# Kernel optimization log

Hardware: AMD Instinct MI355X
Metric: run time of the kernel (lower is better)

Reference implementation:

```python
import jax, jax.numpy as jnp
import numpy as np
from jax import lax

R_WIN = 1
WIN = 2 * R_WIN + 1        # 3
K = WIN * WIN              # 9
STRIDE = 4
LATENT = 128
N_LVL = 2


def _conv_relu(x, w, b):
    # x: (B*S, 3, H, W), w: (128, 3, 7, 7) -> (B*S, 128, H/4, W/4)
    y = lax.conv_general_dilated(x, w, (STRIDE, STRIDE), [(3, 3), (3, 3)],
                                 dimension_numbers=('NCHW', 'OIHW', 'NCHW'))
    return jax.nn.relu(y + b[None, :, None, None])


def _bilinear_sample(fmap, gx, gy):
    # fmap (B,C,H,W); gx,gy (B,P) in [-1,1]; align_corners=True, zeros padding
    B, C, H, W = fmap.shape
    ix = (gx + 1.0) * 0.5 * (W - 1)
    iy = (gy + 1.0) * 0.5 * (H - 1)
    x0 = jnp.floor(ix); y0 = jnp.floor(iy)
    x1 = x0 + 1.0;      y1 = y0 + 1.0
    wx1 = ix - x0; wx0 = 1.0 - wx1
    wy1 = iy - y0; wy0 = 1.0 - wy1

    fm_flat = fmap.reshape(B, C, H * W)

    def corner(xf, yf, wgt):
        valid = (xf >= 0) & (xf <= W - 1) & (yf >= 0) & (yf <= H - 1)
        xi = jnp.clip(xf, 0, W - 1).astype(jnp.int32)
        yi = jnp.clip(yf, 0, H - 1).astype(jnp.int32)
        idx = yi * W + xi                              # (B,P)
        g = jax.vmap(lambda fm, ii: fm[:, ii])(fm_flat, idx)  # (B,C,P)
        return g * (wgt * valid)[:, None, :]

    return (corner(x0, y0, wx0 * wy0) + corner(x1, y0, wx1 * wy0)
            + corner(x0, y1, wx0 * wy1) + corner(x1, y1, wx1 * wy1))


def _sample_features(fmap, pts):
    B, C, H, W = fmap.shape
    N = pts.shape[1]
    lin = jnp.linspace(-R_WIN, R_WIN, WIN)
    dy, dx = jnp.meshgrid(lin, lin, indexing='ij')
    off = jnp.stack([dx / (W - 1) * 2.0, dy / (H - 1) * 2.0], -1).reshape(-1, 2)  # (K,2)
    grid = (pts * 2.0 - 1.0)[:, :, None, :] + off[None, None]   # (B,N,K,2)
    grid = grid.reshape(B, N * K, 2)
    s = _bilinear_sample(fmap, grid[..., 0], grid[..., 1])       # (B,C,N*K)
    return s.reshape(B, C, N, WIN, WIN)


def _l2norm(x, axis):
    return x / jnp.maximum(jnp.linalg.norm(x, axis=axis, keepdims=True), 1e-12)


def _forward(queries, frames, conv_w, conv_b, w1, b1, wp, bp, wv, bv):
    B, S, C, H, W = frames.shape
    N = queries.shape[1]
    x = 2.0 * (frames / 255.0) - 1.0
    fm = _conv_relu(x.reshape(B * S, C, H, W), conv_w, conv_b)
    fm = fm.reshape(B, S, LATENT, H // STRIDE, W // STRIDE)

    pyr = [fm]
    for _ in range(N_LVL - 1):
        fm = lax.reduce_window(fm, 0.0, lax.add, (1, 1, 1, WIN, WIN),
                               (1, 1, 1, WIN, WIN), 'VALID') / float(WIN * WIN)
        pyr.append(fm)

    cur = queries                                   # pred_pos aliases queries in torch
    vis_acc = jnp.zeros((B, N), queries.dtype)
    for i in range(N_LVL):
        f5 = pyr[N_LVL - 1 - i]                     # (B,S,C,h,w) coarse -> fine
        feats = _sample_features(f5[:, 0], cur).reshape(B, LATENT, N, K)
        matches = _sample_features(f5[:, 1], cur).reshape(B, LATENT, N, K)
        fn = _l2norm(feats, 1)
        mn = _l2norm(matches, 1)
        corr = jnp.einsum('bcnh,bcnk->bnhk', fn, mn).reshape(B * N, K * K)
        h = jax.nn.relu(corr @ w1 + b1)
        pred = jax.nn.softmax(h @ wp + bp, axis=-1).reshape(B, N, WIN, WIN)
        vis = jax.nn.sigmoid(h @ wv + bv).reshape(B, N)
        hh, ww = f5.shape[3], f5.shape[4]
        dsx = jnp.linspace(-R_WIN / (ww - 1), R_WIN / (ww - 1), WIN)
        dsy = jnp.linspace(-R_WIN / (hh - 1), R_WIN / (hh - 1), WIN)
        d_x = pred.sum(-1) @ dsx                    # (B,N)
        d_y = pred.sum(-2) @ dsy                    # (B,N)
        cur = jnp.stack([cur[..., 0] + d_x, cur[..., 1] + d_y], -1)
        vis_acc = vis_acc + vis
    return cur, vis_acc / float(N_LVL)


def setup_inputs() -> dict:
    key = jax.random.key(0)
    ks = jax.random.split(key, 8)
    B, S, N, H, W = 2, 2, 8192, 384, 512
    return {
        'queries': jax.random.uniform(ks[0], (B, N, 2), jnp.float32),
        'frames': jax.random.uniform(ks[1], (B, S, 3, H, W), jnp.float32) * 255.0,
        'conv_w': jax.random.normal(ks[2], (128, 3, 7, 7), jnp.float32) * 0.02,
        'conv_b': jnp.zeros((128,), jnp.float32),
        'w1': jax.random.normal(ks[3], (81, 256), jnp.float32) * 0.05,
        'b1': jnp.zeros((256,), jnp.float32),
        'wp': jax.random.normal(ks[4], (256, 9), jnp.float32) * 0.05,
        'bp': jnp.zeros((9,), jnp.float32),
        'wv': jax.random.normal(ks[5], (256, 1), jnp.float32) * 0.05,
        'bv': jnp.zeros((1,), jnp.float32),
    }


def reference(queries, frames, conv_w, conv_b, w1, b1, wp, bp, wv, bv):
    return _forward(queries, frames, conv_w, conv_b, w1, b1, wp, bp, wv, bv)
```

## Files before the change

kernel.cpp:

```cpp
#include <hip/hip_runtime.h>
#include <math.h>

#define NQ 8192
#define NP 16384
#define H_IN 384
#define W_IN 512
#define HH0 96
#define WW0 128
#define HH1 32
#define WW1 42

__global__ void transpose_w_kernel(const float* __restrict__ w, float* __restrict__ wT) {
    int idx = blockIdx.x * 256 + threadIdx.x;
    if (idx < 147 * 128) {
        int tap = idx >> 7;
        int oc  = idx & 127;
        wT[idx] = w[oc * 147 + tap];
    }
}

__global__ __launch_bounds__(256) void conv_kernel(
    const float* __restrict__ frames, const float* __restrict__ wT,
    const float* __restrict__ bias, float* __restrict__ out)
{
    __shared__ float lds[3 * 7 * 260];
    const int bs  = blockIdx.z;
    const int oh  = blockIdx.y;
    const int ow0 = blockIdx.x * 64;
    const int tid = threadIdx.x;

    for (int idx = tid; idx < 3 * 7 * 259; idx += 256) {
        int c   = idx / 1813;
        int rem = idx - c * 1813;
        int kh  = rem / 259;
        int col = rem - kh * 259;
        int gy  = oh * 4 - 3 + kh;
        int gx  = ow0 * 4 - 3 + col;
        float v = 0.0f;
        if (gy >= 0 && gy < H_IN && gx >= 0 && gx < W_IN) {
            float t = frames[((size_t)(bs * 3 + c) * H_IN + gy) * W_IN + gx];
            v = 2.0f * (t / 255.0f) - 1.0f;
        }
        lds[c * 1820 + kh * 260 + col] = v;
    }
    __syncthreads();

    const int oc = tid & 63;
    const int g  = tid >> 6;
    float a0[16], a1[16];
#pragma unroll
    for (int p = 0; p < 16; ++p) { a0[p] = 0.0f; a1[p] = 0.0f; }

#pragma unroll
    for (int c = 0; c < 3; ++c) {
#pragma unroll
        for (int kh = 0; kh < 7; ++kh) {
            const float* row = lds + c * 1820 + kh * 260 + g * 64;
            float w0[7], w1v[7];
#pragma unroll
            for (int kw = 0; kw < 7; ++kw) {
                int tap = (c * 7 + kh) * 7 + kw;
                w0[kw]  = wT[tap * 128 + oc];
                w1v[kw] = wT[tap * 128 + oc + 64];
            }
#pragma unroll
            for (int p = 0; p < 16; ++p) {
                const float4 A  = *(const float4*)(row + p * 4);
                const float4 Bv = *(const float4*)(row + p * 4 + 4);
                float s0 = a0[p], s1 = a1[p];
                s0 = fmaf(A.x,  w0[0], s0);  s1 = fmaf(A.x,  w1v[0], s1);
                s0 = fmaf(A.y,  w0[1], s0);  s1 = fmaf(A.y,  w1v[1], s1);
                s0 = fmaf(A.z,  w0[2], s0);  s1 = fmaf(A.z,  w1v[2], s1);
                s0 = fmaf(A.w,  w0[3], s0);  s1 = fmaf(A.w,  w1v[3], s1);
                s0 = fmaf(Bv.x, w0[4], s0);  s1 = fmaf(Bv.x, w1v[4], s1);
                s0 = fmaf(Bv.y, w0[5], s0);  s1 = fmaf(Bv.y, w1v[5], s1);
                s0 = fmaf(Bv.z, w0[6], s0);  s1 = fmaf(Bv.z, w1v[6], s1);
                a0[p] = s0; a1[p] = s1;
            }
        }
    }

    const float b0  = bias[oc];
    const float b1b = bias[oc + 64];
#pragma unroll
    for (int p = 0; p < 16; ++p) {
        int ow = ow0 + g * 16 + p;
        size_t ob = ((size_t)(bs * HH0 + oh) * WW0 + ow) * 128;
        out[ob + oc]      = fmaxf(a0[p] + b0, 0.0f);
        out[ob + oc + 64] = fmaxf(a1[p] + b1b, 0.0f);
    }
}

__global__ void pool_kernel(const float* __restrict__ in, float* __restrict__ out) {
    int idx = blockIdx.x * 256 + threadIdx.x;
    if (idx >= 4 * HH1 * WW1 * 128) return;
    int c = idx & 127;
    int r = idx >> 7;
    int px = r % WW1; r /= WW1;
    int py = r % HH1;
    int bs = r / HH1;
    float s = 0.0f;
#pragma unroll
    for (int dy = 0; dy < 3; ++dy)
#pragma unroll
        for (int dx = 0; dx < 3; ++dx)
            s += in[(((size_t)bs * HH0 + py * 3 + dy) * WW0 + px * 3 + dx) * 128 + c];
    out[idx] = s / 9.0f;
}

__global__ __launch_bounds__(512) void sample_kernel(
    const float* __restrict__ fm, int hh, int ww,
    const float* __restrict__ cur_in, float* __restrict__ corr_out)
{
    __shared__ float smem[4 * 2400];
    const int tid  = threadIdx.x;
    const int wvi  = tid >> 6;
    const int lane = tid & 63;
    const int ps   = wvi >> 1;
    const int mp   = wvi & 1;
    const int p    = blockIdx.x * 4 + ps;
    const int b    = p >> 13;

    float* fl    = smem + ps * 2400;
    float* ml    = fl + 1188;
    float* inv_s = fl + 2376;

    const float2 pxy = *(const float2*)(cur_in + (size_t)p * 2);
    const float wwm1 = (float)(ww - 1);
    const float hhm1 = (float)(hh - 1);
    const float ix = ((pxy.x * 2.0f - 1.0f) + 1.0f) * 0.5f * wwm1;
    const float iy = ((pxy.y * 2.0f - 1.0f) + 1.0f) * 0.5f * hhm1;
    const float x0 = floorf(ix), y0 = floorf(iy);
    const float fx1 = ix - x0, fx0 = 1.0f - fx1;
    const float fy1 = iy - y0, fy0 = 1.0f - fy1;

    int   cx[4], cy[4];
    float vx[4], vy[4];
#pragma unroll
    for (int j = 0; j < 4; ++j) {
        float xc = x0 + (float)(j - 1);
        vx[j] = (xc >= 0.0f && xc <= wwm1) ? 1.0f : 0.0f;
        cx[j] = (int)fminf(fmaxf(xc, 0.0f), wwm1);
        float yc = y0 + (float)(j - 1);
        vy[j] = (yc >= 0.0f && yc <= hhm1) ? 1.0f : 0.0f;
        cy[j] = (int)fminf(fmaxf(yc, 0.0f), hhm1);
    }
    float cwx[6], cwy[6];
#pragma unroll
    for (int t = 0; t < 3; ++t) {
        cwx[t * 2 + 0] = fx0 * vx[t]; cwx[t * 2 + 1] = fx1 * vx[t + 1];
        cwy[t * 2 + 0] = fy0 * vy[t]; cwy[t * 2 + 1] = fy1 * vy[t + 1];
    }

    {
        const float2* src = (const float2*)fm + (size_t)(b * 2 + mp) * hh * ww * 64;
        float* dst = mp ? ml : fl;
        float2 P[4][4];
#pragma unroll
        for (int j = 0; j < 4; ++j)
#pragma unroll
            for (int i = 0; i < 4; ++i)
                P[j][i] = src[(cy[j] * ww + cx[i]) * 64 + lane];
#pragma unroll
        for (int ky = 0; ky < 3; ++ky)
#pragma unroll
            for (int kx = 0; kx < 3; ++kx) {
                float wA = cwy[ky * 2 + 0] * cwx[kx * 2 + 0];
                float wB = cwy[ky * 2 + 0] * cwx[kx * 2 + 1];
                float wC = cwy[ky * 2 + 1] * cwx[kx * 2 + 0];
                float wD = cwy[ky * 2 + 1] * cwx[kx * 2 + 1];
                float sx = wA * P[ky][kx].x;
                sx = fmaf(wB, P[ky][kx + 1].x, sx);
                sx = fmaf(wC, P[ky + 1][kx].x, sx);
                sx = fmaf(wD, P[ky + 1][kx + 1].x, sx);
                float sy = wA * P[ky][kx].y;
                sy = fmaf(wB, P[ky][kx + 1].y, sy);
                sy = fmaf(wC, P[ky + 1][kx].y, sy);
                sy = fmaf(wD, P[ky + 1][kx + 1].y, sy);
                *(float2*)(dst + (ky * 3 + kx) * 132 + 2 * lane) = make_float2(sx, sy);
            }
    }
    __syncthreads();

    const int e = mp * 64 + lane;
    float s = 0.0f;
    {
        const float *rA, *rB;
        if (e < 81)      { rA = fl + (e / 9) * 132; rB = ml + (e % 9) * 132; }
        else if (e < 90) { rA = fl + (e - 81) * 132; rB = rA; }
        else             { int em = e - 90; if (em > 8) em = 8;
                           rA = ml + em * 132; rB = rA; }
#pragma unroll
        for (int c = 0; c < 128; c += 4) {
            float4 a  = *(const float4*)(rA + c);
            float4 bb = *(const float4*)(rB + c);
            s += a.x * bb.x; s += a.y * bb.y; s += a.z * bb.z; s += a.w * bb.w;
        }
    }
    if (e >= 81 && e < 90)      inv_s[e - 81]     = 1.0f / fmaxf(sqrtf(s), 1e-12f);
    else if (e >= 90 && e < 99) inv_s[e - 90 + 9] = 1.0f / fmaxf(sqrtf(s), 1e-12f);
    __syncthreads();

    if (e < 81)
        corr_out[(size_t)p * 81 + e] = s * inv_s[e / 9] * inv_s[9 + e % 9];
}

__global__ __launch_bounds__(256) void mlp_kernel(
    const float* __restrict__ corr, const float* __restrict__ cur_in,
    const float* __restrict__ w1, const float* __restrict__ b1,
    const float* __restrict__ wp, const float* __restrict__ bp,
    const float* __restrict__ wvw, const float* __restrict__ bvv,
    int hh, int ww,
    float* __restrict__ cur_out,
    const float* __restrict__ vis_in, float* __restrict__ vis_out,
    int is_last)
{
    __shared__ float cls[16 * 81];
    __shared__ float wps[256 * 9];
    __shared__ float wvs[256];
    __shared__ float red[4 * 10 * 16];
    const int tid   = threadIdx.x;
    const int wvi   = tid >> 6;
    const int lane  = tid & 63;
    const int pbase = blockIdx.x * 16;
    const int pl_   = lane & 15;
    const int jg    = wvi * 4 + (lane >> 4);
    const int j0    = jg * 16;

    for (int idx = tid; idx < 16 * 81; idx += 256)
        cls[idx] = corr[(size_t)pbase * 81 + idx];
    for (int idx = tid; idx < 256 * 9; idx += 256)
        wps[idx] = wp[idx];
    if (tid < 256) wvs[tid] = wvw[tid];
    __syncthreads();

    float h[16];
#pragma unroll
    for (int jj = 0; jj < 16; ++jj) h[jj] = b1[j0 + jj];

    const float* crow = cls + pl_ * 81;
    for (int i = 0; i < 81; ++i) {
        const float cv = crow[i];
        const float4* wr = (const float4*)(w1 + i * 256 + j0);
        float4 w4a = wr[0], w4b = wr[1], w4c = wr[2], w4d = wr[3];
        h[0]  = fmaf(cv, w4a.x, h[0]);  h[1]  = fmaf(cv, w4a.y, h[1]);
        h[2]  = fmaf(cv, w4a.z, h[2]);  h[3]  = fmaf(cv, w4a.w, h[3]);
        h[4]  = fmaf(cv, w4b.x, h[4]);  h[5]  = fmaf(cv, w4b.y, h[5]);
        h[6]  = fmaf(cv, w4b.z, h[6]);  h[7]  = fmaf(cv, w4b.w, h[7]);
        h[8]  = fmaf(cv, w4c.x, h[8]);  h[9]  = fmaf(cv, w4c.y, h[9]);
        h[10] = fmaf(cv, w4c.z, h[10]); h[11] = fmaf(cv, w4c.w, h[11]);
        h[12] = fmaf(cv, w4d.x, h[12]); h[13] = fmaf(cv, w4d.y, h[13]);
        h[14] = fmaf(cv, w4d.z, h[14]); h[15] = fmaf(cv, w4d.w, h[15]);
    }

    float pl10[10];
#pragma unroll
    for (int o = 0; o < 10; ++o) pl10[o] = 0.0f;
#pragma unroll
    for (int jj = 0; jj < 16; ++jj) {
        float hv = fmaxf(h[jj], 0.0f);
        const float* wr = wps + (j0 + jj) * 9;
#pragma unroll
        for (int o = 0; o < 9; ++o) pl10[o] = fmaf(hv, wr[o], pl10[o]);
        pl10[9] = fmaf(hv, wvs[j0 + jj], pl10[9]);
    }
#pragma unroll
    for (int o = 0; o < 10; ++o) {
        pl10[o] += __shfl_xor(pl10[o], 16);
        pl10[o] += __shfl_xor(pl10[o], 32);
    }
    if ((lane >> 4) == 0) {
#pragma unroll
        for (int o = 0; o < 10; ++o)
            red[(wvi * 10 + o) * 16 + pl_] = pl10[o];
    }
    __syncthreads();

    if (tid < 16) {
        const int p = pbase + tid;
        float fo[10];
#pragma unroll
        for (int o = 0; o < 10; ++o) {
            float v = red[o * 16 + tid];
            v += red[(10 + o) * 16 + tid];
            v += red[(20 + o) * 16 + tid];
            v += red[(30 + o) * 16 + tid];
            fo[o] = v;
        }
        float lg[9];
#pragma unroll
        for (int o = 0; o < 9; ++o) lg[o] = fo[o] + bp[o];
        float mx = lg[0];
#pragma unroll
        for (int o = 1; o < 9; ++o) mx = fmaxf(mx, lg[o]);
        float ex[9], sum = 0.0f;
#pragma unroll
        for (int o = 0; o < 9; ++o) { ex[o] = expf(lg[o] - mx); sum += ex[o]; }
#pragma unroll
        for (int o = 0; o < 9; ++o) ex[o] = ex[o] / sum;

        float vis = 1.0f / (1.0f + expf(-(fo[9] + bvv[0])));

        const float wwm1 = (float)(ww - 1);
        const float hhm1 = (float)(hh - 1);
        const float ax = 1.0f / wwm1;
        const float ay = 1.0f / hhm1;
        float r0 = ex[0] + ex[1] + ex[2];
        float r1 = ex[3] + ex[4] + ex[5];
        float r2 = ex[6] + ex[7] + ex[8];
        float c0 = ex[0] + ex[3] + ex[6];
        float c1 = ex[1] + ex[4] + ex[7];
        float c2 = ex[2] + ex[5] + ex[8];
        float dx = r0 * (-ax) + r1 * 0.0f + r2 * ax;
        float dy = c0 * (-ay) + c1 * 0.0f + c2 * ay;

        float2 pq = *(const float2*)(cur_in + (size_t)p * 2);
        *(float2*)(cur_out + (size_t)p * 2) = make_float2(pq.x + dx, pq.y + dy);
        vis_out[p] = is_last ? (vis_in[p] + vis) * 0.5f : vis;
    }
}

extern "C" void kernel_launch(void* const* d_in, const int* in_sizes, int n_in,
                              void* d_out, int out_size, void* d_ws, size_t ws_size,
                              hipStream_t stream) {
    (void)in_sizes; (void)n_in; (void)out_size; (void)ws_size;
    const float* queries = (const float*)d_in[0];
    const float* frames  = (const float*)d_in[1];
    const float* conv_w  = (const float*)d_in[2];
    const float* conv_b  = (const float*)d_in[3];
    const float* w1      = (const float*)d_in[4];
    const float* b1      = (const float*)d_in[5];
    const float* wp      = (const float*)d_in[6];
    const float* bp      = (const float*)d_in[7];
    const float* wvw     = (const float*)d_in[8];
    const float* bvv     = (const float*)d_in[9];
    float* out = (float*)d_out;

    float* ws     = (float*)d_ws;
    float* fm0    = ws;
    float* fm1    = fm0 + 6291456;
    float* wT     = fm1 + 688128;
    float* cur_ws = wT + 18816;
    float* vis_ws = cur_ws + 32768;
    float* corrws = vis_ws + 16384;

    transpose_w_kernel<<<74, 256, 0, stream>>>(conv_w, wT);
    conv_kernel<<<dim3(2, HH0, 4), 256, 0, stream>>>(frames, wT, conv_b, fm0);
    pool_kernel<<<2688, 256, 0, stream>>>(fm0, fm1);

    sample_kernel<<<4096, 512, 0, stream>>>(fm1, HH1, WW1, queries, corrws);
    mlp_kernel<<<1024, 256, 0, stream>>>(corrws, queries, w1, b1, wp, bp, wvw, bvv,
                                         HH1, WW1, cur_ws, nullptr, vis_ws, 0);
    sample_kernel<<<4096, 512, 0, stream>>>(fm0, HH0, WW0, cur_ws, corrws);
    mlp_kernel<<<1024, 256, 0, stream>>>(corrws, cur_ws, w1, b1, wp, bp, wvw, bvv,
                                         HH0, WW0, out, vis_ws, out + 32768, 1);
}
```

Measured before the change: 269.6 us.

## Register-block MLP hidden layer with split-K over inputs and shared-memory reduction

Rewrites the MLP kernel's first layer so each thread keeps a 10x8 slice of w1 in registers and computes an 8-point by 8-hidden tile. The 81 input features are split across eight thread groups, and partial sums are reduced through shuffles and a shared-memory buffer. The point-major correlation tile is transposed in shared memory so points can be loaded as float4. This removes the repeated per-iteration global reads of w1 and raises FMA density. In exchange it adds register pressure, a large shared-memory reduction buffer and extra barriers, and it also adds a min-blocks launch bound.

```diff
diff --git a/kernel.cpp b/kernel.cpp
--- a/kernel.cpp
+++ b/kernel.cpp
@@ -205,7 +205,7 @@
         corr_out[(size_t)p * 81 + e] = s * inv_s[e / 9] * inv_s[9 + e % 9];
 }
 
-__global__ __launch_bounds__(256) void mlp_kernel(
+__global__ __launch_bounds__(256, 2) void mlp_kernel(
     const float* __restrict__ corr, const float* __restrict__ cur_in,
     const float* __restrict__ w1, const float* __restrict__ b1,
     const float* __restrict__ wp, const float* __restrict__ bp,
@@ -215,108 +215,157 @@
     const float* __restrict__ vis_in, float* __restrict__ vis_out,
     int is_last)
 {
-    __shared__ float cls[16 * 81];
-    __shared__ float wps[256 * 9];
-    __shared__ float wvs[256];
-    __shared__ float red[4 * 10 * 16];
-    const int tid   = threadIdx.x;
-    const int wvi   = tid >> 6;
-    const int lane  = tid & 63;
-    const int pbase = blockIdx.x * 16;
-    const int pl_   = lane & 15;
-    const int jg    = wvi * 4 + (lane >> 4);
-    const int j0    = jg * 16;
-
-    for (int idx = tid; idx < 16 * 81; idx += 256)
-        cls[idx] = corr[(size_t)pbase * 81 + idx];
-    for (int idx = tid; idx < 256 * 9; idx += 256)
-        wps[idx] = wp[idx];
-    if (tid < 256) wvs[tid] = wvw[tid];
+    __shared__ float cls_t[81 * 16];
+    __shared__ float wps[256 * 9 + 256];
+    __shared__ float hred[4 * 8 * 32 * 12];
+    const int tid    = threadIdx.x;
+    const int wvi    = tid >> 6;
+    const int lane   = tid & 63;
+    const int jsl    = tid & 31;
+    const int j0     = jsl * 8;
+    const int ksl    = tid >> 5;
+    const int kstart = ksl * 10;
+    const int pbase  = blockIdx.x * 16;
+
+    for (int idx = tid; idx < 16 * 81; idx += 256) {
+        int pt = idx / 81, i = idx - pt * 81;
+        cls_t[i * 16 + pt] = corr[(size_t)pbase * 81 + idx];
+    }
+    for (int idx = tid; idx < 2304; idx += 256) wps[idx] = wp[idx];
+    wps[2304 + tid] = wvw[tid];
+
+    float w1r[10][8];
+#pragma unroll
+    for (int ii = 0; ii < 10; ++ii) {
+        const float4* wr = (const float4*)(w1 + (kstart + ii) * 256 + j0);
+        float4 a = wr[0], b = wr[1];
+        w1r[ii][0] = a.x; w1r[ii][1] = a.y; w1r[ii][2] = a.z; w1r[ii][3] = a.w;
+        w1r[ii][4] = b.x; w1r[ii][5] = b.y; w1r[ii][6] = b.z; w1r[ii][7] = b.w;
+    }
+    float w1e[8] = {0, 0, 0, 0, 0, 0, 0, 0};
+    if (ksl == 7) {
+        const float4* wr = (const float4*)(w1 + 80 * 256 + j0);
+        float4 a = wr[0], b = wr[1];
+        w1e[0] = a.x; w1e[1] = a.y; w1e[2] = a.z; w1e[3] = a.w;
+        w1e[4] = b.x; w1e[5] = b.y; w1e[6] = b.z; w1e[7] = b.w;
+    }
     __syncthreads();
 
-    float h[16];
-#pragma unroll
-    for (int jj = 0; jj < 16; ++jj) h[jj] = b1[j0 + jj];
-
-    const float* crow = cls + pl_ * 81;
-    for (int i = 0; i < 81; ++i) {
-        const float cv = crow[i];
-        const float4* wr = (const float4*)(w1 + i * 256 + j0);
-        float4 w4a = wr[0], w4b = wr[1], w4c = wr[2], w4d = wr[3];
-        h[0]  = fmaf(cv, w4a.x, h[0]);  h[1]  = fmaf(cv, w4a.y, h[1]);
-        h[2]  = fmaf(cv, w4a.z, h[2]);  h[3]  = fmaf(cv, w4a.w, h[3]);
-        h[4]  = fmaf(cv, w4b.x, h[4]);  h[5]  = fmaf(cv, w4b.y, h[5]);
-        h[6]  = fmaf(cv, w4b.z, h[6]);  h[7]  = fmaf(cv, w4b.w, h[7]);
-        h[8]  = fmaf(cv, w4c.x, h[8]);  h[9]  = fmaf(cv, w4c.y, h[9]);
-        h[10] = fmaf(cv, w4c.z, h[10]); h[11] = fmaf(cv, w4c.w, h[11]);
-        h[12] = fmaf(cv, w4d.x, h[12]); h[13] = fmaf(cv, w4d.y, h[13]);
-        h[14] = fmaf(cv, w4d.z, h[14]); h[15] = fmaf(cv, w4d.w, h[15]);
-    }
-
-    float pl10[10];
-#pragma unroll
-    for (int o = 0; o < 10; ++o) pl10[o] = 0.0f;
-#pragma unroll
-    for (int jj = 0; jj < 16; ++jj) {
-        float hv = fmaxf(h[jj], 0.0f);
-        const float* wr = wps + (j0 + jj) * 9;
-#pragma unroll
-        for (int o = 0; o < 9; ++o) pl10[o] = fmaf(hv, wr[o], pl10[o]);
-        pl10[9] = fmaf(hv, wvs[j0 + jj], pl10[9]);
-    }
-#pragma unroll
-    for (int o = 0; o < 10; ++o) {
-        pl10[o] += __shfl_xor(pl10[o], 16);
-        pl10[o] += __shfl_xor(pl10[o], 32);
-    }
-    if ((lane >> 4) == 0) {
-#pragma unroll
-        for (int o = 0; o < 10; ++o)
-            red[(wvi * 10 + o) * 16 + pl_] = pl10[o];
-    }
-    __syncthreads();
-
-    if (tid < 16) {
-        const int p = pbase + tid;
-        float fo[10];
+    for (int t = 0; t < 2; ++t) {
+        const int pt0 = t * 8;
+        float h[8][8];
+#pragma unroll
+        for (int p = 0; p < 8; ++p)
+#pragma unroll
+            for (int j = 0; j < 8; ++j) h[p][j] = 0.0f;
+
+#pragma unroll
+        for (int ii = 0; ii < 10; ++ii) {
+            const int i = kstart + ii;
+            const float4 cva = *(const float4*)(cls_t + i * 16 + pt0);
+            const float4 cvb = *(const float4*)(cls_t + i * 16 + pt0 + 4);
+            const float cv[8] = {cva.x, cva.y, cva.z, cva.w,
+                                 cvb.x, cvb.y, cvb.z, cvb.w};
+#pragma unroll
+            for (int p = 0; p < 8; ++p)
+#pragma unroll
+                for (int j = 0; j < 8; ++j)
+                    h[p][j] = fmaf(cv[p], w1r[ii][j], h[p][j]);
+        }
+        if (ksl == 7) {
+            const float4 cva = *(const float4*)(cls_t + 80 * 16 + pt0);
+            const float4 cvb = *(const float4*)(cls_t + 80 * 16 + pt0 + 4);
+            const float cv[8] = {cva.x, cva.y, cva.z, cva.w,
+                                 cvb.x, cvb.y, cvb.z, cvb.w};
+#pragma unroll
+            for (int p = 0; p < 8; ++p)
+#pragma unroll
+                for (int j = 0; j < 8; ++j)
+                    h[p][j] = fmaf(cv[p], w1e[j], h[p][j]);
+        }
+
+#pragma unroll
+        for (int p = 0; p < 8; ++p)
+#pragma unroll
+            for (int j = 0; j < 8; ++j)
+                h[p][j] += __shfl_xor(h[p][j], 32);
+
+        if (lane < 32) {
+#pragma unroll
+            for (int p = 0; p < 8; ++p) {
+                float* dst = hred + ((wvi * 8 + p) * 32 + jsl) * 12;
+                *(float4*)(dst)     = make_float4(h[p][0], h[p][1], h[p][2], h[p][3]);
+                *(float4*)(dst + 4) = make_float4(h[p][4], h[p][5], h[p][6], h[p][7]);
+            }
+        }
+        __syncthreads();
+
+        const int pth = ksl;
+        const int jc  = jsl;
+        float hf[8];
+#pragma unroll
+        for (int j = 0; j < 8; ++j) hf[j] = 0.0f;
+#pragma unroll
+        for (int w = 0; w < 4; ++w) {
+            const float* src = hred + ((w * 8 + pth) * 32 + jc) * 12;
+            const float4 a = *(const float4*)(src);
+            const float4 b = *(const float4*)(src + 4);
+            hf[0] += a.x; hf[1] += a.y; hf[2] += a.z; hf[3] += a.w;
+            hf[4] += b.x; hf[5] += b.y; hf[6] += b.z; hf[7] += b.w;
+        }
+
+        float pl10[10];
+#pragma unroll
+        for (int o = 0; o < 10; ++o) pl10[o] = 0.0f;
+#pragma unroll
+        for (int j = 0; j < 8; ++j) {
+            const float hv = fmaxf(hf[j] + b1[jc * 8 + j], 0.0f);
+            const float* wr = wps + (jc * 8 + j) * 9;
+#pragma unroll
+            for (int o = 0; o < 9; ++o) pl10[o] = fmaf(hv, wr[o], pl10[o]);
+            pl10[9] = fmaf(hv, wps[2304 + jc * 8 + j], pl10[9]);
+        }
 #pragma unroll
         for (int o = 0; o < 10; ++o) {
-            float v = red[o * 16 + tid];
-            v += red[(10 + o) * 16 + tid];
-            v += red[(20 + o) * 16 + tid];
-            v += red[(30 + o) * 16 + tid];
-            fo[o] = v;
-        }
-        float lg[9];
-#pragma unroll
-        for (int o = 0; o < 9; ++o) lg[o] = fo[o] + bp[o];
-        float mx = lg[0];
-#pragma unroll
-        for (int o = 1; o < 9; ++o) mx = fmaxf(mx, lg[o]);
-        float ex[9], sum = 0.0f;
-#pragma unroll
-        for (int o = 0; o < 9; ++o) { ex[o] = expf(lg[o] - mx); sum += ex[o]; }
-#pragma unroll
-        for (int o = 0; o < 9; ++o) ex[o] = ex[o] / sum;
-
-        float vis = 1.0f / (1.0f + expf(-(fo[9] + bvv[0])));
-
-        const float wwm1 = (float)(ww - 1);
-        const float hhm1 = (float)(hh - 1);
-        const float ax = 1.0f / wwm1;
-        const float ay = 1.0f / hhm1;
-        float r0 = ex[0] + ex[1] + ex[2];
-        float r1 = ex[3] + ex[4] + ex[5];
-        float r2 = ex[6] + ex[7] + ex[8];
-        float c0 = ex[0] + ex[3] + ex[6];
-        float c1 = ex[1] + ex[4] + ex[7];
-        float c2 = ex[2] + ex[5] + ex[8];
-        float dx = r0 * (-ax) + r1 * 0.0f + r2 * ax;
-        float dy = c0 * (-ay) + c1 * 0.0f + c2 * ay;
-
-        float2 pq = *(const float2*)(cur_in + (size_t)p * 2);
-        *(float2*)(cur_out + (size_t)p * 2) = make_float2(pq.x + dx, pq.y + dy);
-        vis_out[p] = is_last ? (vis_in[p] + vis) * 0.5f : vis;
+            pl10[o] += __shfl_xor(pl10[o], 1);
+            pl10[o] += __shfl_xor(pl10[o], 2);
+            pl10[o] += __shfl_xor(pl10[o], 4);
+            pl10[o] += __shfl_xor(pl10[o], 8);
+            pl10[o] += __shfl_xor(pl10[o], 16);
+        }
+
+        if (jc == 0) {
+            const int p = pbase + pt0 + pth;
+            float lg[9];
+#pragma unroll
+            for (int o = 0; o < 9; ++o) lg[o] = pl10[o] + bp[o];
+            float mx = lg[0];
+#pragma unroll
+            for (int o = 1; o < 9; ++o) mx = fmaxf(mx, lg[o]);
+            float ex[9], sum = 0.0f;
+#pragma unroll
+            for (int o = 0; o < 9; ++o) { ex[o] = expf(lg[o] - mx); sum += ex[o]; }
+#pragma unroll
+            for (int o = 0; o < 9; ++o) ex[o] = ex[o] / sum;
+
+            const float vis = 1.0f / (1.0f + expf(-(pl10[9] + bvv[0])));
+
+            const float wwm1 = (float)(ww - 1);
+            const float hhm1 = (float)(hh - 1);
+            const float ax = 1.0f / wwm1;
+            const float ay = 1.0f / hhm1;
+            const float r0 = ex[0] + ex[1] + ex[2];
+            const float r2 = ex[6] + ex[7] + ex[8];
+            const float c0 = ex[0] + ex[3] + ex[6];
+            const float c2 = ex[2] + ex[5] + ex[8];
+            const float dx = r0 * (-ax) + r2 * ax;
+            const float dy = c0 * (-ay) + c2 * ay;
+
+            const float2 pq = *(const float2*)(cur_in + (size_t)p * 2);
+            *(float2*)(cur_out + (size_t)p * 2) = make_float2(pq.x + dx, pq.y + dy);
+            vis_out[p] = is_last ? (vis_in[p] + vis) * 0.5f : vis;
+        }
+        __syncthreads();
     }
 }
 
```

New measurement: 267.1 us. Within noise of the previous version (-0.9%).

## Retile MLP kernel: two points per thread, reduce via warp shuffles

Applied to the files above, without the earlier changes.

Restructures the MLP kernel's work split so each thread computes 8 hidden units for 2 points. Previously each thread handled 16 hidden units for 1 point. The correlation tile is stored transposed in shared memory so a thread loads both points' values with one float2. The partial outputs are reduced across 32 lanes with shuffles, removing the shared-memory reduction buffer and the second barrier. This reuses each w1 load across two points, at the cost of more shuffle instructions and per-thread registers.

```diff
diff --git a/kernel.cpp b/kernel.cpp
--- a/kernel.cpp
+++ b/kernel.cpp
@@ -215,108 +215,131 @@
     const float* __restrict__ vis_in, float* __restrict__ vis_out,
     int is_last)
 {
-    __shared__ float cls[16 * 81];
+    __shared__ float cls_t[81 * 18];
     __shared__ float wps[256 * 9];
     __shared__ float wvs[256];
-    __shared__ float red[4 * 10 * 16];
     const int tid   = threadIdx.x;
-    const int wvi   = tid >> 6;
-    const int lane  = tid & 63;
+    const int jg    = tid & 31;
+    const int pg    = tid >> 5;
     const int pbase = blockIdx.x * 16;
-    const int pl_   = lane & 15;
-    const int jg    = wvi * 4 + (lane >> 4);
-    const int j0    = jg * 16;
-
-    for (int idx = tid; idx < 16 * 81; idx += 256)
-        cls[idx] = corr[(size_t)pbase * 81 + idx];
-    for (int idx = tid; idx < 256 * 9; idx += 256)
-        wps[idx] = wp[idx];
-    if (tid < 256) wvs[tid] = wvw[tid];
+
+    for (int idx = tid; idx < 16 * 81; idx += 256) {
+        int pt = idx / 81, i = idx - pt * 81;
+        cls_t[i * 18 + pt] = corr[(size_t)pbase * 81 + idx];
+    }
+    for (int idx = tid; idx < 2304; idx += 256) wps[idx] = wp[idx];
+    wvs[tid] = wvw[tid];
     __syncthreads();
 
-    float h[16];
-#pragma unroll
-    for (int jj = 0; jj < 16; ++jj) h[jj] = b1[j0 + jj];
-
-    const float* crow = cls + pl_ * 81;
-    for (int i = 0; i < 81; ++i) {
-        const float cv = crow[i];
-        const float4* wr = (const float4*)(w1 + i * 256 + j0);
-        float4 w4a = wr[0], w4b = wr[1], w4c = wr[2], w4d = wr[3];
-        h[0]  = fmaf(cv, w4a.x, h[0]);  h[1]  = fmaf(cv, w4a.y, h[1]);
-        h[2]  = fmaf(cv, w4a.z, h[2]);  h[3]  = fmaf(cv, w4a.w, h[3]);
-        h[4]  = fmaf(cv, w4b.x, h[4]);  h[5]  = fmaf(cv, w4b.y, h[5]);
-        h[6]  = fmaf(cv, w4b.z, h[6]);  h[7]  = fmaf(cv, w4b.w, h[7]);
-        h[8]  = fmaf(cv, w4c.x, h[8]);  h[9]  = fmaf(cv, w4c.y, h[9]);
-        h[10] = fmaf(cv, w4c.z, h[10]); h[11] = fmaf(cv, w4c.w, h[11]);
-        h[12] = fmaf(cv, w4d.x, h[12]); h[13] = fmaf(cv, w4d.y, h[13]);
-        h[14] = fmaf(cv, w4d.z, h[14]); h[15] = fmaf(cv, w4d.w, h[15]);
-    }
-
-    float pl10[10];
-#pragma unroll
-    for (int o = 0; o < 10; ++o) pl10[o] = 0.0f;
-#pragma unroll
-    for (int jj = 0; jj < 16; ++jj) {
-        float hv = fmaxf(h[jj], 0.0f);
-        const float* wr = wps + (j0 + jj) * 9;
-#pragma unroll
-        for (int o = 0; o < 9; ++o) pl10[o] = fmaf(hv, wr[o], pl10[o]);
-        pl10[9] = fmaf(hv, wvs[j0 + jj], pl10[9]);
+    float h0[8], h1[8];
+    {
+        const float4* bp4 = (const float4*)(b1 + jg * 8);
+        float4 ba = bp4[0], bb = bp4[1];
+        h0[0] = ba.x; h0[1] = ba.y; h0[2] = ba.z; h0[3] = ba.w;
+        h0[4] = bb.x; h0[5] = bb.y; h0[6] = bb.z; h0[7] = bb.w;
+#pragma unroll
+        for (int j = 0; j < 8; ++j) h1[j] = h0[j];
+    }
+
+    const float* wbase = w1 + jg * 8;
+    const float* cvbase = cls_t + pg * 2;
+    for (int i = 0; i < 81; i += 3) {
+        const float4 a0 = *(const float4*)(wbase + (i    ) * 256);
+        const float4 a1 = *(const float4*)(wbase + (i    ) * 256 + 4);
+        const float4 b0 = *(const float4*)(wbase + (i + 1) * 256);
+        const float4 b1q = *(const float4*)(wbase + (i + 1) * 256 + 4);
+        const float4 c0 = *(const float4*)(wbase + (i + 2) * 256);
+        const float4 c1 = *(const float4*)(wbase + (i + 2) * 256 + 4);
+        const float2 cvA = *(const float2*)(cvbase + (i    ) * 18);
+        const float2 cvB = *(const float2*)(cvbase + (i + 1) * 18);
+        const float2 cvC = *(const float2*)(cvbase + (i + 2) * 18);
+        h0[0] = fmaf(cvA.x, a0.x, h0[0]); h1[0] = fmaf(cvA.y, a0.x, h1[0]);
+        h0[1] = fmaf(cvA.x, a0.y, h0[1]); h1[1] = fmaf(cvA.y, a0.y, h1[1]);
+        h0[2] = fmaf(cvA.x, a0.z, h0[2]); h1[2] = fmaf(cvA.y, a0.z, h1[2]);
+        h0[3] = fmaf(cvA.x, a0.w, h0[3]); h1[3] = fmaf(cvA.y, a0.w, h1[3]);
+        h0[4] = fmaf(cvA.x, a1.x, h0[4]); h1[4] = fmaf(cvA.y, a1.x, h1[4]);
+        h0[5] = fmaf(cvA.x, a1.y, h0[5]); h1[5] = fmaf(cvA.y, a1.y, h1[5]);
+        h0[6] = fmaf(cvA.x, a1.z, h0[6]); h1[6] = fmaf(cvA.y, a1.z, h1[6]);
+        h0[7] = fmaf(cvA.x, a1.w, h0[7]); h1[7] = fmaf(cvA.y, a1.w, h1[7]);
+        h0[0] = fmaf(cvB.x, b0.x, h0[0]); h1[0] = fmaf(cvB.y, b0.x, h1[0]);
+        h0[1] = fmaf(cvB.x, b0.y, h0[1]); h1[1] = fmaf(cvB.y, b0.y, h1[1]);
+        h0[2] = fmaf(cvB.x, b0.z, h0[2]); h1[2] = fmaf(cvB.y, b0.z, h1[2]);
+        h0[3] = fmaf(cvB.x, b0.w, h0[3]); h1[3] = fmaf(cvB.y, b0.w, h1[3]);
+        h0[4] = fmaf(cvB.x, b1q.x, h0[4]); h1[4] = fmaf(cvB.y, b1q.x, h1[4]);
+        h0[5] = fmaf(cvB.x, b1q.y, h0[5]); h1[5] = fmaf(cvB.y, b1q.y, h1[5]);
+        h0[6] = fmaf(cvB.x, b1q.z, h0[6]); h1[6] = fmaf(cvB.y, b1q.z, h1[6]);
+        h0[7] = fmaf(cvB.x, b1q.w, h0[7]); h1[7] = fmaf(cvB.y, b1q.w, h1[7]);
+        h0[0] = fmaf(cvC.x, c0.x, h0[0]); h1[0] = fmaf(cvC.y, c0.x, h1[0]);
+        h0[1] = fmaf(cvC.x, c0.y, h0[1]); h1[1] = fmaf(cvC.y, c0.y, h1[1]);
+        h0[2] = fmaf(cvC.x, c0.z, h0[2]); h1[2] = fmaf(cvC.y, c0.z, h1[2]);
+        h0[3] = fmaf(cvC.x, c0.w, h0[3]); h1[3] = fmaf(cvC.y, c0.w, h1[3]);
+        h0[4] = fmaf(cvC.x, c1.x, h0[4]); h1[4] = fmaf(cvC.y, c1.x, h1[4]);
+        h0[5] = fmaf(cvC.x, c1.y, h0[5]); h1[5] = fmaf(cvC.y, c1.y, h1[5]);
+        h0[6] = fmaf(cvC.x, c1.z, h0[6]); h1[6] = fmaf(cvC.y, c1.z, h1[6]);
+        h0[7] = fmaf(cvC.x, c1.w, h0[7]); h1[7] = fmaf(cvC.y, c1.w, h1[7]);
+    }
+
+    float pl0[10], pl1[10];
+#pragma unroll
+    for (int o = 0; o < 10; ++o) { pl0[o] = 0.0f; pl1[o] = 0.0f; }
+#pragma unroll
+    for (int j = 0; j < 8; ++j) {
+        const float hv0 = fmaxf(h0[j], 0.0f);
+        const float hv1 = fmaxf(h1[j], 0.0f);
+        const float* wr = wps + (jg * 8 + j) * 9;
+#pragma unroll
+        for (int o = 0; o < 9; ++o) {
+            const float wv = wr[o];
+            pl0[o] = fmaf(hv0, wv, pl0[o]);
+            pl1[o] = fmaf(hv1, wv, pl1[o]);
+        }
+        const float wvv = wvs[jg * 8 + j];
+        pl0[9] = fmaf(hv0, wvv, pl0[9]);
+        pl1[9] = fmaf(hv1, wvv, pl1[9]);
     }
 #pragma unroll
     for (int o = 0; o < 10; ++o) {
-        pl10[o] += __shfl_xor(pl10[o], 16);
-        pl10[o] += __shfl_xor(pl10[o], 32);
-    }
-    if ((lane >> 4) == 0) {
-#pragma unroll
-        for (int o = 0; o < 10; ++o)
-            red[(wvi * 10 + o) * 16 + pl_] = pl10[o];
-    }
-    __syncthreads();
-
-    if (tid < 16) {
-        const int p = pbase + tid;
-        float fo[10];
-#pragma unroll
-        for (int o = 0; o < 10; ++o) {
-            float v = red[o * 16 + tid];
-            v += red[(10 + o) * 16 + tid];
-            v += red[(20 + o) * 16 + tid];
-            v += red[(30 + o) * 16 + tid];
-            fo[o] = v;
-        }
-        float lg[9];
-#pragma unroll
-        for (int o = 0; o < 9; ++o) lg[o] = fo[o] + bp[o];
-        float mx = lg[0];
-#pragma unroll
-        for (int o = 1; o < 9; ++o) mx = fmaxf(mx, lg[o]);
-        float ex[9], sum = 0.0f;
-#pragma unroll
-        for (int o = 0; o < 9; ++o) { ex[o] = expf(lg[o] - mx); sum += ex[o]; }
-#pragma unroll
-        for (int o = 0; o < 9; ++o) ex[o] = ex[o] / sum;
-
-        float vis = 1.0f / (1.0f + expf(-(fo[9] + bvv[0])));
-
+        pl0[o] += __shfl_xor(pl0[o], 1);  pl1[o] += __shfl_xor(pl1[o], 1);
+        pl0[o] += __shfl_xor(pl0[o], 2);  pl1[o] += __shfl_xor(pl1[o], 2);
+        pl0[o] += __shfl_xor(pl0[o], 4);  pl1[o] += __shfl_xor(pl1[o], 4);
+        pl0[o] += __shfl_xor(pl0[o], 8);  pl1[o] += __shfl_xor(pl1[o], 8);
+        pl0[o] += __shfl_xor(pl0[o], 16); pl1[o] += __shfl_xor(pl1[o], 16);
+    }
+
+    if (jg == 0) {
         const float wwm1 = (float)(ww - 1);
         const float hhm1 = (float)(hh - 1);
         const float ax = 1.0f / wwm1;
         const float ay = 1.0f / hhm1;
-        float r0 = ex[0] + ex[1] + ex[2];
-        float r1 = ex[3] + ex[4] + ex[5];
-        float r2 = ex[6] + ex[7] + ex[8];
-        float c0 = ex[0] + ex[3] + ex[6];
-        float c1 = ex[1] + ex[4] + ex[7];
-        float c2 = ex[2] + ex[5] + ex[8];
-        float dx = r0 * (-ax) + r1 * 0.0f + r2 * ax;
-        float dy = c0 * (-ay) + c1 * 0.0f + c2 * ay;
-
-        float2 pq = *(const float2*)(cur_in + (size_t)p * 2);
-        *(float2*)(cur_out + (size_t)p * 2) = make_float2(pq.x + dx, pq.y + dy);
-        vis_out[p] = is_last ? (vis_in[p] + vis) * 0.5f : vis;
+#pragma unroll
+        for (int t = 0; t < 2; ++t) {
+            const float* fo = t ? pl1 : pl0;
+            const int p = pbase + pg * 2 + t;
+            float lg[9];
+#pragma unroll
+            for (int o = 0; o < 9; ++o) lg[o] = fo[o] + bp[o];
+            float mx = lg[0];
+#pragma unroll
+            for (int o = 1; o < 9; ++o) mx = fmaxf(mx, lg[o]);
+            float ex[9], sum = 0.0f;
+#pragma unroll
+            for (int o = 0; o < 9; ++o) { ex[o] = expf(lg[o] - mx); sum += ex[o]; }
+#pragma unroll
+            for (int o = 0; o < 9; ++o) ex[o] = ex[o] / sum;
+
+            const float vis = 1.0f / (1.0f + expf(-(fo[9] + bvv[0])));
+
+            const float r0 = ex[0] + ex[1] + ex[2];
+            const float r2 = ex[6] + ex[7] + ex[8];
+            const float c0 = ex[0] + ex[3] + ex[6];
+            const float c2 = ex[2] + ex[5] + ex[8];
+            const float dx = r0 * (-ax) + r2 * ax;
+            const float dy = c0 * (-ay) + c2 * ay;
+
+            const float2 pq = *(const float2*)(cur_in + (size_t)p * 2);
+            *(float2*)(cur_out + (size_t)p * 2) = make_float2(pq.x + dx, pq.y + dy);
+            vis_out[p] = is_last ? (vis_in[p] + vis) * 0.5f : vis;
+        }
     }
 }
 
```

Result: faster. 251.6 us (-6.7%).
